# Kernel tuning notes

Measured on AMD Instinct MI355X. Metric: run time of the kernel, lower is better.

Reference implementation:

```python
import jax, jax.numpy as jnp
import numpy as np

N, E, B = 65536, 524288, 256
FEAT, EMB, NH, NB, NC = 64, 128, 4, 2, 4
OUT = EMB // NH
SLOPE = 0.01  # LeakyReLU negative_slope used everywhere in the module


def lrelu(x):
    return jnp.where(x > 0, x, SLOPE * x)


def seg_softmax(logits, seg, nseg, mask):
    # PyG softmax(src, batch): exp(x - segment_max) / (segment_sum + 1e-16)
    z = jnp.where(mask, logits, -jnp.inf)
    m = jax.ops.segment_max(z, seg, num_segments=nseg)
    m = jnp.where(jnp.isfinite(m), m, 0.0)
    e = jnp.exp(z - m[seg])
    s = jax.ops.segment_sum(e, seg, num_segments=nseg)
    return e / (s[seg] + 1e-16)


def topk_pool(x, seg, w, min_score, nseg):
    # PyG TopKPooling with min_score: score = softmax(x.w, batch);
    # keep nodes with score > min(min_score, per-graph max - 1e-7); x_out = x*score.
    score = x @ w  # [N]
    sm = seg_softmax(score, seg, nseg, jnp.ones(score.shape, bool))
    smax = jax.ops.segment_max(sm, seg, num_segments=nseg)
    thr = jnp.minimum(smax - 1e-7, min_score)
    keep = sm > thr[seg]
    xp = jnp.where(keep[:, None], x * sm[:, None], 0.0)
    return xp, keep


def graph_conv_max(x, src, dst, emask, Wrel, Wroot, b, n):
    # PyG GraphConv(aggr='max'): out = Wrel @ max_{j in N(i)} x_j + Wroot @ x_i + b
    msg = jnp.where(emask[:, None], x[src], -jnp.inf)  # [E, d]
    agg = jax.ops.segment_max(msg, dst, num_segments=n)
    agg = jnp.where(jnp.isfinite(agg), agg, 0.0)  # nodes with no in-edges -> 0 (PyG scatter fill)
    return agg @ Wrel.T + x @ Wroot.T + b


def batchnorm(x, g, b):
    # training-mode BatchNorm1d: batch statistics, biased variance, eps=1e-5
    mu = x.mean(0)
    var = x.var(0)
    return g * (x - mu) * jax.lax.rsqrt(var + 1e-5) + b


def setup_inputs() -> dict:
    key = jax.random.key(0)
    ks = jax.random.split(key, 16)
    s_feat = np.float32(1.0 / np.sqrt(FEAT))
    s_emb = np.float32(1.0 / np.sqrt(EMB))
    return {
        "x": jax.random.normal(ks[0], (N, FEAT), jnp.float32),
        "edge_index": jax.random.randint(ks[1], (2, E), 0, N, jnp.int32),
        "batch": (jnp.arange(N, dtype=jnp.int32) // (N // B)).astype(jnp.int32),
        "W_rel0": jax.random.normal(ks[2], (EMB, FEAT), jnp.float32) * s_feat,
        "W_root0": jax.random.normal(ks[3], (EMB, FEAT), jnp.float32) * s_feat,
        "b0": jnp.zeros((EMB,), jnp.float32),
        "bn0_g": jnp.ones((EMB,), jnp.float32),
        "bn0_b": jnp.zeros((EMB,), jnp.float32),
        "blk_pool_w": jax.random.normal(ks[4], (NB, NH, EMB), jnp.float32) * s_emb,
        "blk_Wrel": jax.random.normal(ks[5], (NB, NH, OUT, EMB), jnp.float32) * s_emb,
        "blk_Wroot": jax.random.normal(ks[6], (NB, NH, OUT, EMB), jnp.float32) * s_emb,
        "blk_b": jnp.zeros((NB, NH, OUT), jnp.float32),
        "blk_bn_g": jnp.ones((NB, EMB), jnp.float32),
        "blk_bn_b": jnp.zeros((NB, EMB), jnp.float32),
        "cls_pool_w": jax.random.normal(ks[7], (NC, EMB), jnp.float32) * s_emb,
        "cls_gW1": jax.random.normal(ks[8], (NC, EMB, EMB), jnp.float32) * s_emb,
        "cls_gb1": jnp.zeros((NC, EMB), jnp.float32),
        "cls_gW2": jax.random.normal(ks[9], (NC, EMB), jnp.float32) * s_emb,
        "cls_gb2": jnp.zeros((NC,), jnp.float32),
        "cls_fW1": jax.random.normal(ks[10], (NC, EMB, EMB), jnp.float32) * s_emb,
        "cls_fb1": jnp.zeros((NC, EMB), jnp.float32),
        "cls_fW2": jax.random.normal(ks[11], (NC, EMB), jnp.float32) * s_emb,
        "cls_fb2": jnp.zeros((NC,), jnp.float32),
        "batch_size": B,
    }


def reference(x, edge_index, batch, W_rel0, W_root0, b0, bn0_g, bn0_b,
              blk_pool_w, blk_Wrel, blk_Wroot, blk_b, blk_bn_g, blk_bn_b,
              cls_pool_w, cls_gW1, cls_gb1, cls_gW2, cls_gb2,
              cls_fW1, cls_fb1, cls_fW2, cls_fb2, batch_size):
    n = x.shape[0]
    src, dst = edge_index[0], edge_index[1]
    all_e = jnp.ones(src.shape, bool)
    # conv0 -> leaky_relu -> bn0
    h = lrelu(graph_conv_max(x, src, dst, all_e, W_rel0, W_root0, b0, n))
    cur = batchnorm(h, bn0_g, bn0_b)
    # multi-head blocks: pool (min_score=0.7) -> GraphConv(max) per head, scatter
    # back to original node slots, concat heads, bn, residual 0.5*(x + 0.5*bn(new))
    for bi in range(NB):
        heads = []
        for hi in range(NH):
            xp, keep = topk_pool(cur, batch, blk_pool_w[bi, hi], 0.7, batch_size)
            emask = keep[src] & keep[dst]
            o = lrelu(graph_conv_max(xp, src, dst, emask,
                                     blk_Wrel[bi, hi], blk_Wroot[bi, hi],
                                     blk_b[bi, hi], n))
            heads.append(jnp.where(keep[:, None], o, 0.0))
        new = batchnorm(jnp.concatenate(heads, axis=-1), blk_bn_g[bi], blk_bn_b[bi])
        cur = 0.5 * (cur + 0.5 * new)
    # classification heads: pool (min_score=0.8) -> GlobalAttention -> MLP -> 1
    outs = []
    for c in range(NC):
        xp, keep = topk_pool(cur, batch, cls_pool_w[c], 0.8, batch_size)
        gate = lrelu(xp @ cls_gW1[c].T + cls_gb1[c]) @ cls_gW2[c] + cls_gb2[c]  # [N]
        a = seg_softmax(gate, batch, batch_size, keep)
        pooled = jax.ops.segment_sum(a[:, None] * xp, batch, num_segments=batch_size)  # [B, EMB]
        y = lrelu(pooled @ cls_fW1[c].T + cls_fb1[c]) @ cls_fW2[c] + cls_fb2[c]  # [B]
        outs.append(y)
    logits = jnp.stack(outs, axis=-1)  # [B, NC]
    return jax.nn.log_softmax(logits, axis=-1)
```

## Files before the change

kernel.cpp:

```cpp
#include <hip/hip_runtime.h>
#include <math.h>

#define NN 65536
#define NE 524288
#define NG 256
#define SLOPE 0.01f

__device__ __forceinline__ float lrelu(float v){ return v > 0.f ? v : SLOPE*v; }

__device__ __forceinline__ float blockMax4(float v, float* s4){
  #pragma unroll
  for(int o=32;o>0;o>>=1) v = fmaxf(v, __shfl_down(v, o, 64));
  int t = threadIdx.x;
  __syncthreads();
  if((t&63)==0) s4[t>>6] = v;
  __syncthreads();
  return fmaxf(fmaxf(s4[0], s4[1]), fmaxf(s4[2], s4[3]));
}
__device__ __forceinline__ float blockSum4(float v, float* s4){
  #pragma unroll
  for(int o=32;o>0;o>>=1) v += __shfl_down(v, o, 64);
  int t = threadIdx.x;
  __syncthreads();
  if((t&63)==0) s4[t>>6] = v;
  __syncthreads();
  return (s4[0]+s4[1])+(s4[2]+s4[3]);
}

__global__ __launch_bounds__(256) void k_count(const int* __restrict__ ei, int* __restrict__ deg){
  int e = blockIdx.x*256 + threadIdx.x;
  if(e < NE) atomicAdd(&deg[ei[NE + e]], 1);
}

__global__ __launch_bounds__(1024) void k_scan(const int* __restrict__ deg,
      int* __restrict__ offs, int* __restrict__ cursor){
  __shared__ int part[1024];
  int t = threadIdx.x;
  int base = t*64;
  int s=0;
  for(int i=0;i<64;i++) s += deg[base+i];
  part[t]=s;
  __syncthreads();
  for(int off=1; off<1024; off<<=1){
    int v = (t>=off)? part[t-off] : 0;
    __syncthreads();
    part[t] += v;
    __syncthreads();
  }
  int run = (t==0)? 0 : part[t-1];
  for(int i=0;i<64;i++){
    int d = deg[base+i];
    offs[base+i] = run; cursor[base+i] = run;
    run += d;
  }
  if(t==1023) offs[NN] = run;
}

__global__ __launch_bounds__(256) void k_scatter(const int* __restrict__ ei,
      int* __restrict__ cursor, int* __restrict__ csr){
  int e = blockIdx.x*256 + threadIdx.x;
  if(e < NE){
    int d = ei[NE + e];
    int p = atomicAdd(&cursor[d], 1);
    csr[p] = ei[e];
  }
}

__global__ __launch_bounds__(256) void k_agg0(const float* __restrict__ x,
    const int* __restrict__ offs, const int* __restrict__ csr, float* __restrict__ agg0){
  int tid = blockIdx.x*256 + threadIdx.x;
  int node = tid>>4, q = tid&15;
  int e0 = offs[node], e1 = offs[node+1];
  float4 acc = make_float4(0.f,0.f,0.f,0.f);
  if(e0 < e1){
    acc = make_float4(-INFINITY,-INFINITY,-INFINITY,-INFINITY);
    int e = e0;
    for(; e+3 < e1; e += 4){
      int s0 = csr[e], s1 = csr[e+1], s2 = csr[e+2], s3 = csr[e+3];
      float4 v0 = ((const float4*)x)[s0*16 + q];
      float4 v1 = ((const float4*)x)[s1*16 + q];
      float4 v2 = ((const float4*)x)[s2*16 + q];
      float4 v3 = ((const float4*)x)[s3*16 + q];
      acc.x=fmaxf(acc.x,fmaxf(fmaxf(v0.x,v1.x),fmaxf(v2.x,v3.x)));
      acc.y=fmaxf(acc.y,fmaxf(fmaxf(v0.y,v1.y),fmaxf(v2.y,v3.y)));
      acc.z=fmaxf(acc.z,fmaxf(fmaxf(v0.z,v1.z),fmaxf(v2.z,v3.z)));
      acc.w=fmaxf(acc.w,fmaxf(fmaxf(v0.w,v1.w),fmaxf(v2.w,v3.w)));
    }
    for(; e < e1; e++){
      int s0 = csr[e];
      float4 v0 = ((const float4*)x)[s0*16 + q];
      acc.x=fmaxf(acc.x,v0.x); acc.y=fmaxf(acc.y,v0.y);
      acc.z=fmaxf(acc.z,v0.z); acc.w=fmaxf(acc.w,v0.w);
    }
  }
  ((float4*)agg0)[node*16 + q] = acc;
}

__global__ __launch_bounds__(256, 2) void k_conv0mm(
    const float* __restrict__ agg0, const float* __restrict__ x,
    const float* __restrict__ Wrel, const float* __restrict__ Wroot,
    const float* __restrict__ b0, float* __restrict__ cur,
    float* __restrict__ bnsum, float* __restrict__ bnsq){
  __shared__ float4 As[2048];
  __shared__ float4 Ws[2048];
  const int t = threadIdx.x;
  const int tn = t & 15;
  const int tc = t >> 4;
  float acc[8][8];
  #pragma unroll
  for(int i=0;i<8;i++)
    #pragma unroll
    for(int j=0;j<8;j++) acc[i][j]=0.f;

  const size_t tileoff = (size_t)blockIdx.x * 8192;
  #pragma unroll 1
  for(int ch=0; ch<2; ch++){
    const float4* gA = (const float4*)((ch==0? agg0 : x) + tileoff);
    const float4* gW = (const float4*)(ch==0? Wrel : Wroot);
    __syncthreads();
    #pragma unroll
    for(int i=0;i<8;i++){
      int idx = t + i*256;
      int n = idx>>4, k4 = idx&15;
      int sw = n*16 + ((k4 + (n>>3))&15);
      As[sw] = gA[idx];
      Ws[sw] = gW[idx];
    }
    __syncthreads();
    #pragma unroll 4
    for(int k4=0;k4<16;k4++){
      float4 a4[8], w4[8];
      #pragma unroll
      for(int i=0;i<8;i++) a4[i] = As[(tn*8+i)*16 + ((k4+tn)&15)];
      #pragma unroll
      for(int i=0;i<8;i++) w4[i] = Ws[(tc*8+i)*16 + ((k4+tc)&15)];
      #pragma unroll
      for(int i=0;i<8;i++)
        #pragma unroll
        for(int j=0;j<8;j++){
          acc[i][j] = fmaf(a4[i].x, w4[j].x, acc[i][j]);
          acc[i][j] = fmaf(a4[i].y, w4[j].y, acc[i][j]);
          acc[i][j] = fmaf(a4[i].z, w4[j].z, acc[i][j]);
          acc[i][j] = fmaf(a4[i].w, w4[j].w, acc[i][j]);
        }
    }
  }

  float bj[8];
  #pragma unroll
  for(int j=0;j<8;j++) bj[j] = b0[tc*8+j];
  float cs[8], cq[8];
  #pragma unroll
  for(int j=0;j<8;j++){ cs[j]=0.f; cq[j]=0.f; }
  const int nbase = blockIdx.x*128;
  #pragma unroll
  for(int i=0;i<8;i++){
    int node = nbase + tn*8 + i;
    float v[8];
    #pragma unroll
    for(int j=0;j<8;j++){
      v[j] = lrelu(acc[i][j] + bj[j]);
      cs[j] += v[j]; cq[j] += v[j]*v[j];
    }
    float4 o0 = make_float4(v[0],v[1],v[2],v[3]);
    float4 o1 = make_float4(v[4],v[5],v[6],v[7]);
    ((float4*)cur)[node*32 + tc*2 + 0] = o0;
    ((float4*)cur)[node*32 + tc*2 + 1] = o1;
  }
  __syncthreads();
  float* reds = (float*)As;
  float* redq = (float*)Ws;
  #pragma unroll
  for(int j=0;j<8;j++){
    reds[(tc*8+j)*16 + tn] = cs[j];
    redq[(tc*8+j)*16 + tn] = cq[j];
  }
  __syncthreads();
  if(t<128){
    float S=0.f, Q=0.f;
    #pragma unroll
    for(int i=0;i<16;i++){ S += reds[t*16+i]; Q += redq[t*16+i]; }
    atomicAdd(&bnsum[t], S);
    atomicAdd(&bnsq[t], Q);
  }
}

__global__ __launch_bounds__(256) void k_pool(const float* __restrict__ cur,
    const float* __restrict__ pw, float minscore,
    float* __restrict__ sm4, unsigned char* __restrict__ keep,
    int* __restrict__ cnt, int* __restrict__ wl,
    const float* __restrict__ bnsum, const float* __restrict__ bnsq,
    const float* __restrict__ gg, int fold){
  __shared__ __align__(16) float w[4][128];
  __shared__ float red[4];
  __shared__ float scv[128];
  int t = threadIdx.x, g = blockIdx.x;
  if(t<128){
    float sv = 1.f;
    if(fold){
      float mu = bnsum[t]*(1.0f/NN);
      float var = bnsq[t]*(1.0f/NN) - mu*mu;
      sv = gg[t]*rsqrtf(var+1e-5f);
    }
    scv[t] = sv;
  }
  __syncthreads();
  for(int i=t;i<512;i+=256) w[i>>7][i&127] = pw[i]*scv[i&127];
  __syncthreads();
  int n = g*256 + t;
  const float4* row = (const float4*)(cur + (size_t)n*128);
  float sc[4] = {0.f,0.f,0.f,0.f};
  for(int k=0;k<32;k++){
    float4 v = row[k];
    #pragma unroll
    for(int h=0;h<4;h++){
      const float4 wv = *(const float4*)&w[h][k*4];
      sc[h] += v.x*wv.x + v.y*wv.y + v.z*wv.z + v.w*wv.w;
    }
  }
  float4 smout;
  unsigned kb = 0;
  #pragma unroll 1
  for(int h=0;h<4;h++){
    float m = blockMax4(sc[h], red);
    float e = expf(sc[h]-m);
    float ssum = blockSum4(e, red);
    float sm = e/(ssum + 1e-16f);
    float smax = blockMax4(sm, red);
    float thr = fminf(smax - 1e-7f, minscore);
    ((float*)&smout)[h] = sm;
    if(sm > thr){
      kb |= (1u<<h);
      int p = atomicAdd(cnt, 1);
      wl[p] = (h<<16) | n;
    }
  }
  ((float4*)sm4)[n] = smout;
  keep[n] = (unsigned char)kb;
}

__global__ __launch_bounds__(256) void k_blockconv(const float* __restrict__ cur,
    const int* __restrict__ offs, const int* __restrict__ csr,
    const unsigned char* __restrict__ keep, const float* __restrict__ sm4,
    const int* __restrict__ cnt, const int* __restrict__ wl,
    const float* __restrict__ Wrel, const float* __restrict__ Wroot,
    const float* __restrict__ bias,
    float* __restrict__ onew, float* __restrict__ bnsum, float* __restrict__ bnsq,
    const float* __restrict__ bns0, const float* __restrict__ bnq0,
    const float* __restrict__ g0, const float* __restrict__ b0bn, int fold){
  __shared__ __align__(16) float aggs[8][128];
  __shared__ __align__(16) float xps[8][128];
  __shared__ __align__(16) float scv[128];
  __shared__ __align__(16) float ofv[128];
  const int t = threadIdx.x, grp = t>>5, lane = t&31;
  if(t<128){
    float sv = 1.f, ov = 0.f;
    if(fold){
      float mu = bns0[t]*(1.0f/NN);
      float var = bnq0[t]*(1.0f/NN) - mu*mu;
      sv = g0[t]*rsqrtf(var+1e-5f);
      ov = b0bn[t] - mu*sv;
    }
    scv[t]=sv; ofv[t]=ov;
  }
  __syncthreads();
  const float4 s4l = *(const float4*)&scv[lane*4];
  const float4 o4l = *(const float4*)&ofv[lane*4];
  const int total = *cnt;
  for(int item = blockIdx.x*8 + grp; item < total; item += gridDim.x*8){
    const int wv = wl[item];
    const int h = wv>>16, n = wv & 0xFFFF;
    const float smn = sm4[n*4+h];
    const int e0 = offs[n], e1 = offs[n+1];
    float4 acc = make_float4(-INFINITY,-INFINITY,-INFINITY,-INFINITY);
    bool any = false;
    for(int e=e0;e<e1;e++){
      int s = csr[e];
      if((keep[s]>>h)&1){
        any = true;
        float sv = sm4[s*4+h];
        float4 v = ((const float4*)cur)[s*32 + lane];
        v.x = (v.x*s4l.x + o4l.x)*sv; v.y = (v.y*s4l.y + o4l.y)*sv;
        v.z = (v.z*s4l.z + o4l.z)*sv; v.w = (v.w*s4l.w + o4l.w)*sv;
        acc.x = fmaxf(acc.x, v.x); acc.y = fmaxf(acc.y, v.y);
        acc.z = fmaxf(acc.z, v.z); acc.w = fmaxf(acc.w, v.w);
      }
    }
    if(!any) acc = make_float4(0.f,0.f,0.f,0.f);
    *(float4*)&aggs[grp][lane*4] = acc;
    float4 xv = ((const float4*)cur)[n*32 + lane];
    xv.x = (xv.x*s4l.x + o4l.x)*smn; xv.y = (xv.y*s4l.y + o4l.y)*smn;
    xv.z = (xv.z*s4l.z + o4l.z)*smn; xv.w = (xv.w*s4l.w + o4l.w)*smn;
    *(float4*)&xps[grp][lane*4] = xv;
    const float* Wr = Wrel  + (size_t)(h*32+lane)*128;
    const float* Wo = Wroot + (size_t)(h*32+lane)*128;
    float o = bias[h*32+lane];
    for(int k=0;k<32;k++){
      float4 a  = *(const float4*)&aggs[grp][k*4];
      float4 xx = *(const float4*)&xps[grp][k*4];
      float4 wr = ((const float4*)Wr)[k];
      float4 wo = ((const float4*)Wo)[k];
      o += a.x*wr.x + a.y*wr.y + a.z*wr.z + a.w*wr.w;
      o += xx.x*wo.x + xx.y*wo.y + xx.z*wo.z + xx.w*wo.w;
    }
    o = lrelu(o);
    onew[(size_t)n*128 + h*32 + lane] = o;
    atomicAdd(&bnsum[h*32+lane], o);
    atomicAdd(&bnsq[h*32+lane], o*o);
  }
}

__global__ __launch_bounds__(256) void k_updatepool(float* __restrict__ cur,
    const float* __restrict__ onew, const unsigned char* __restrict__ keepin,
    const float* __restrict__ bnsum, const float* __restrict__ bnsq,
    const float* __restrict__ gg, const float* __restrict__ bb,
    const float* __restrict__ bns0, const float* __restrict__ bnq0,
    const float* __restrict__ g0, const float* __restrict__ b0bn,
    const float* __restrict__ pw, float minscore,
    float* __restrict__ sm4, unsigned char* __restrict__ keepout,
    int* __restrict__ cnt, int* __restrict__ wl){
  __shared__ __align__(16) float sc1[128], of1[128], sc0[128], of0[128];
  __shared__ __align__(16) float w[4][128];
  __shared__ float red[4];
  const int t = threadIdx.x, g = blockIdx.x;
  if(t<128){
    float mu = bnsum[t]*(1.0f/NN);
    float var = bnsq[t]*(1.0f/NN) - mu*mu;
    float s = gg[t]*rsqrtf(var+1e-5f);
    sc1[t]=s; of1[t]=bb[t]-mu*s;
    float mu0 = bns0[t]*(1.0f/NN);
    float var0 = bnq0[t]*(1.0f/NN) - mu0*mu0;
    float s0v = g0[t]*rsqrtf(var0+1e-5f);
    sc0[t]=s0v; of0[t]=b0bn[t]-mu0*s0v;
  }
  for(int i=t;i<512;i+=256) w[i>>7][i&127] = pw[i];
  __syncthreads();
  const int n = g*256 + t;
  const unsigned kb_in = keepin[n];
  float sc[4] = {0.f,0.f,0.f,0.f};
  for(int k=0;k<32;k++){
    int h = k>>3;
    float4 v = ((const float4*)cur)[n*32 + k];
    float4 nv = make_float4(0.f,0.f,0.f,0.f);
    if((kb_in>>h)&1) nv = ((const float4*)onew)[n*32 + k];
    float4 s1 = *(const float4*)&sc1[k*4];
    float4 o1 = *(const float4*)&of1[k*4];
    float4 s0 = *(const float4*)&sc0[k*4];
    float4 o0 = *(const float4*)&of0[k*4];
    v.x = 0.5f*(s0.x*v.x + o0.x) + 0.25f*(s1.x*nv.x + o1.x);
    v.y = 0.5f*(s0.y*v.y + o0.y) + 0.25f*(s1.y*nv.y + o1.y);
    v.z = 0.5f*(s0.z*v.z + o0.z) + 0.25f*(s1.z*nv.z + o1.z);
    v.w = 0.5f*(s0.w*v.w + o0.w) + 0.25f*(s1.w*nv.w + o1.w);
    ((float4*)cur)[n*32 + k] = v;
    #pragma unroll
    for(int h2=0;h2<4;h2++){
      const float4 wv = *(const float4*)&w[h2][k*4];
      sc[h2] += v.x*wv.x + v.y*wv.y + v.z*wv.z + v.w*wv.w;
    }
  }
  float4 smout;
  unsigned kb = 0;
  #pragma unroll 1
  for(int h=0;h<4;h++){
    float m = blockMax4(sc[h], red);
    float e = expf(sc[h]-m);
    float ssum = blockSum4(e, red);
    float sm = e/(ssum + 1e-16f);
    float smax = blockMax4(sm, red);
    float thr = fminf(smax - 1e-7f, minscore);
    ((float*)&smout)[h] = sm;
    if(sm > thr){
      kb |= (1u<<h);
      int p = atomicAdd(cnt, 1);
      wl[p] = (h<<16) | n;
    }
  }
  ((float4*)sm4)[n] = smout;
  keepout[n] = (unsigned char)kb;
}

__global__ __launch_bounds__(256) void k_updatecls(float* __restrict__ cur,
    const float* __restrict__ onew, const unsigned char* __restrict__ keepin,
    const float* __restrict__ bnsum, const float* __restrict__ bnsq,
    const float* __restrict__ gg, const float* __restrict__ bb,
    const float* __restrict__ pw,
    const float* __restrict__ gW1, const float* __restrict__ gb1,
    const float* __restrict__ gW2, const float* __restrict__ gb2,
    const float* __restrict__ fW1, const float* __restrict__ fb1,
    const float* __restrict__ fW2, const float* __restrict__ fb2,
    float* __restrict__ out){
  __shared__ __align__(16) float sc1[128], of1[128];
  __shared__ __align__(16) float w[4][128];
  __shared__ float red[4];
  __shared__ int keptL[256];
  __shared__ float keptS[256];
  __shared__ float gateL[256];
  __shared__ __align__(16) float xk[128];
  __shared__ __align__(16) float pooled[128];
  __shared__ float yv[4];
  __shared__ int nkept;
  const int t = threadIdx.x, g = blockIdx.x;
  if(t<128){
    float mu = bnsum[t]*(1.0f/NN);
    float var = bnsq[t]*(1.0f/NN) - mu*mu;
    float s = gg[t]*rsqrtf(var+1e-5f);
    sc1[t]=s; of1[t]=bb[t]-mu*s;
  }
  for(int i=t;i<512;i+=256) w[i>>7][i&127] = pw[i];
  __syncthreads();
  const int n = g*256 + t;
  const unsigned kb_in = keepin[n];
  float sc4[4] = {0.f,0.f,0.f,0.f};
  for(int k=0;k<32;k++){
    int h = k>>3;
    float4 v = ((const float4*)cur)[n*32 + k];
    float4 nv = make_float4(0.f,0.f,0.f,0.f);
    if((kb_in>>h)&1) nv = ((const float4*)onew)[n*32 + k];
    float4 s1 = *(const float4*)&sc1[k*4];
    float4 o1 = *(const float4*)&of1[k*4];
    v.x = 0.5f*v.x + 0.25f*(s1.x*nv.x + o1.x);
    v.y = 0.5f*v.y + 0.25f*(s1.y*nv.y + o1.y);
    v.z = 0.5f*v.z + 0.25f*(s1.z*nv.z + o1.z);
    v.w = 0.5f*v.w + 0.25f*(s1.w*nv.w + o1.w);
    ((float4*)cur)[n*32 + k] = v;
    #pragma unroll
    for(int c=0;c<4;c++){
      const float4 wv = *(const float4*)&w[c][k*4];
      sc4[c] += v.x*wv.x + v.y*wv.y + v.z*wv.z + v.w*wv.w;
    }
  }
  __syncthreads();
  #pragma unroll 1
  for(int c=0;c<4;c++){
    float m = blockMax4(sc4[c], red);
    float e = expf(sc4[c]-m);
    float ssum = blockSum4(e, red);
    float sm = e/(ssum+1e-16f);
    float smax = blockMax4(sm, red);
    float thr = fminf(smax - 1e-7f, 0.8f);
    if(t==0) nkept = 0;
    __syncthreads();
    if(sm > thr){
      int p = atomicAdd(&nkept,1);
      keptL[p]=t; keptS[p]=sm;
    }
    __syncthreads();
    const int K = nkept;
    for(int k=0;k<K;k++){
      int ln = keptL[k]; float sv = keptS[k];
      if(t<32){
        float4 v = ((const float4*)(cur + (size_t)(g*256+ln)*128))[t];
        v.x*=sv; v.y*=sv; v.z*=sv; v.w*=sv;
        *(float4*)&xk[t*4] = v;
      }
      __syncthreads();
      float part = 0.f;
      if(t<128){
        const float* W = gW1 + (size_t)c*16384 + (size_t)t*128;
        float a = gb1[c*128+t];
        for(int f=0;f<32;f++){
          float4 xv = *(const float4*)&xk[f*4];
          float4 wv = ((const float4*)W)[f];
          a += xv.x*wv.x + xv.y*wv.y + xv.z*wv.z + xv.w*wv.w;
        }
        part = lrelu(a) * gW2[c*128+t];
      }
      float gs = blockSum4(part, red);
      if(t==0) gateL[k] = gs + gb2[c];
      __syncthreads();
    }
    float gv = (t<K)? gateL[t] : -INFINITY;
    float gm = blockMax4(gv, red);
    float ge = (t<K)? expf(gv-gm) : 0.f;
    float gsum = blockSum4(ge, red);
    if(t<K) gateL[t] = ge/(gsum+1e-16f);
    __syncthreads();
    if(t<128){
      float acc = 0.f;
      for(int k=0;k<K;k++)
        acc += gateL[k]*keptS[k]*cur[(size_t)(g*256+keptL[k])*128 + t];
      pooled[t]=acc;
    }
    __syncthreads();
    float part2=0.f;
    if(t<128){
      const float* F = fW1 + (size_t)c*16384 + (size_t)t*128;
      float a = fb1[c*128+t];
      for(int f=0;f<32;f++){
        float4 xv = *(const float4*)&pooled[f*4];
        float4 wv = ((const float4*)F)[f];
        a += xv.x*wv.x + xv.y*wv.y + xv.z*wv.z + xv.w*wv.w;
      }
      part2 = lrelu(a) * fW2[c*128+t];
    }
    float ysum = blockSum4(part2, red);
    if(t==0) yv[c] = ysum + fb2[c];
    __syncthreads();
  }
  if(t<4){
    float m = fmaxf(fmaxf(yv[0],yv[1]), fmaxf(yv[2],yv[3]));
    float l = logf(expf(yv[0]-m)+expf(yv[1]-m)+expf(yv[2]-m)+expf(yv[3]-m));
    out[g*4+t] = yv[t] - m - l;
  }
}

extern "C" void kernel_launch(void* const* d_in, const int* in_sizes, int n_in,
                              void* d_out, int out_size, void* d_ws, size_t ws_size,
                              hipStream_t stream){
  (void)in_sizes; (void)n_in; (void)out_size; (void)ws_size;
  const float* x     = (const float*)d_in[0];
  const int*   ei    = (const int*)d_in[1];
  const float* Wrel0 = (const float*)d_in[3];
  const float* Wroot0= (const float*)d_in[4];
  const float* b0    = (const float*)d_in[5];
  const float* bn0g  = (const float*)d_in[6];
  const float* bn0b  = (const float*)d_in[7];
  const float* bpw   = (const float*)d_in[8];
  const float* bWrel = (const float*)d_in[9];
  const float* bWroot= (const float*)d_in[10];
  const float* bbv   = (const float*)d_in[11];
  const float* bbng  = (const float*)d_in[12];
  const float* bbnb  = (const float*)d_in[13];
  const float* cpw   = (const float*)d_in[14];
  const float* gW1   = (const float*)d_in[15];
  const float* gb1   = (const float*)d_in[16];
  const float* gW2   = (const float*)d_in[17];
  const float* gb2   = (const float*)d_in[18];
  const float* fW1   = (const float*)d_in[19];
  const float* fb1   = (const float*)d_in[20];
  const float* fW2   = (const float*)d_in[21];
  const float* fb2   = (const float*)d_in[22];

  char* ws = (char*)d_ws;
  float* cur   = (float*)(ws + 0);
  float* onew  = (float*)(ws + 33554432ull);
  float* agg0  = onew;
  int*   csr   = (int*)(ws + 67108864ull);
  float* sm4   = (float*)(ws + 69206016ull);
  int*   wl    = (int*)(ws + 70254592ull);
  int*   offs  = (int*)(ws + 71303168ull);
  int*   cursor= (int*)(ws + 71565568ull);
  unsigned char* keep = (unsigned char*)(ws + 71827712ull);
  char*  Z     = ws + 71893248ull;
  int*   deg   = (int*)Z;
  float* bnsum0= (float*)(Z + 262144);
  float* bnsq0 = (float*)(Z + 262656);
  float* bnA   = (float*)(Z + 263168);
  float* bqA   = (float*)(Z + 263680);
  float* bnB   = (float*)(Z + 264192);
  float* bqB   = (float*)(Z + 264704);
  int*   cnt0  = (int*)(Z + 265216);
  int*   cnt1  = (int*)(Z + 265220);

  hipMemsetAsync(Z, 0, 265224, stream);

  k_count  <<<2048,256,0,stream>>>(ei, deg);
  k_scan   <<<1,1024,0,stream>>>(deg, offs, cursor);
  k_scatter<<<2048,256,0,stream>>>(ei, cursor, csr);

  k_agg0    <<<4096,256,0,stream>>>(x, offs, csr, agg0);
  k_conv0mm <<<512,256,0,stream>>>(agg0, x, Wrel0, Wroot0, b0, cur, bnsum0, bnsq0);

  k_pool     <<<256,256,0,stream>>>(cur, bpw, 0.7f, sm4, keep, cnt0, wl,
                                    bnsum0, bnsq0, bn0g, 1);
  k_blockconv<<<256,256,0,stream>>>(cur, offs, csr, keep, sm4, cnt0, wl,
                                    bWrel, bWroot, bbv, onew, bnA, bqA,
                                    bnsum0, bnsq0, bn0g, bn0b, 1);

  k_updatepool<<<256,256,0,stream>>>(cur, onew, keep, bnA, bqA, bbng, bbnb,
                                     bnsum0, bnsq0, bn0g, bn0b,
                                     bpw + 512, 0.7f, sm4, keep, cnt1, wl);

  k_blockconv<<<256,256,0,stream>>>(cur, offs, csr, keep, sm4, cnt1, wl,
                                    bWrel + 16384, bWroot + 16384, bbv + 128, onew, bnB, bqB,
                                    bnsum0, bnsq0, bn0g, bn0b, 0);

  k_updatecls<<<256,256,0,stream>>>(cur, onew, keep, bnB, bqB, bbng + 128, bbnb + 128,
                                    cpw, gW1, gb1, gW2, gb2, fW1, fb1, fW2, fb2,
                                    (float*)d_out);
}
```

Before: 443.5 us.

## Split pool/update kernels into wide streaming score pass plus per-graph selection

Replaces the per-node (one thread per 128-float row) update+score loops with a streaming kernel launched with 8192 blocks where each thread handles one float4, and the four head scores come from warp shuffle reductions. The segment softmax and top-k selection then run in a separate small kernel that reads the precomputed scores. The intent is coalesced memory access and far more parallelism than 256 blocks, which were bandwidth-starved with strided row reads. The cost is extra kernel launches and a scores round trip through global memory; the scores buffer aliases sm4, which k_poolsel reads and then overwrites, so an added __syncthreads guards that.

```diff
diff --git a/kernel.cpp b/kernel.cpp
--- a/kernel.cpp
+++ b/kernel.cpp
@@ -185,45 +185,90 @@
   }
 }
 
-__global__ __launch_bounds__(256) void k_pool(const float* __restrict__ cur,
-    const float* __restrict__ pw, float minscore,
-    float* __restrict__ sm4, unsigned char* __restrict__ keep,
-    int* __restrict__ cnt, int* __restrict__ wl,
-    const float* __restrict__ bnsum, const float* __restrict__ bnsq,
-    const float* __restrict__ gg, int fold){
+template<int MODE>
+__global__ __launch_bounds__(256) void k_stream(
+    float* __restrict__ cur, const float* __restrict__ onew,
+    const unsigned char* __restrict__ keepin,
+    const float* __restrict__ bnsA, const float* __restrict__ bnqA,
+    const float* __restrict__ g1, const float* __restrict__ b1,
+    const float* __restrict__ bns0, const float* __restrict__ bnq0,
+    const float* __restrict__ g0, const float* __restrict__ b0bn,
+    const float* __restrict__ pw, float* __restrict__ scores){
   __shared__ __align__(16) float w[4][128];
+  __shared__ __align__(16) float sc1[128], of1[128], sc0[128], of0[128];
+  const int t = threadIdx.x;
+  if(t<128){
+    if(MODE>=1){
+      float mu = bnsA[t]*(1.0f/NN);
+      float var = bnqA[t]*(1.0f/NN) - mu*mu;
+      float s = g1[t]*rsqrtf(var+1e-5f);
+      sc1[t]=s; of1[t]=b1[t]-mu*s;
+    }
+    if(MODE<=1){
+      float mu0 = bns0[t]*(1.0f/NN);
+      float var0 = bnq0[t]*(1.0f/NN) - mu0*mu0;
+      float s0 = g0[t]*rsqrtf(var0+1e-5f);
+      sc0[t]=s0; of0[t]=b0bn[t]-mu0*s0;
+    }
+  }
+  __syncthreads();
+  for(int i=t;i<512;i+=256){
+    float wv = pw[i];
+    if(MODE==0) wv *= sc0[i&127];
+    w[i>>7][i&127]=wv;
+  }
+  __syncthreads();
+  const int tid = blockIdx.x*256 + t;
+  const int n = tid>>5, k = tid&31;
+  float4 v = ((const float4*)cur)[tid];
+  if(MODE>=1){
+    const int h = k>>3;
+    float4 nv = make_float4(0.f,0.f,0.f,0.f);
+    if((keepin[n]>>h)&1) nv = ((const float4*)onew)[tid];
+    float4 s1 = *(const float4*)&sc1[k*4];
+    float4 o1 = *(const float4*)&of1[k*4];
+    if(MODE==1){
+      float4 s0 = *(const float4*)&sc0[k*4];
+      float4 o0 = *(const float4*)&of0[k*4];
+      v.x = 0.5f*(s0.x*v.x+o0.x) + 0.25f*(s1.x*nv.x+o1.x);
+      v.y = 0.5f*(s0.y*v.y+o0.y) + 0.25f*(s1.y*nv.y+o1.y);
+      v.z = 0.5f*(s0.z*v.z+o0.z) + 0.25f*(s1.z*nv.z+o1.z);
+      v.w = 0.5f*(s0.w*v.w+o0.w) + 0.25f*(s1.w*nv.w+o1.w);
+    } else {
+      v.x = 0.5f*v.x + 0.25f*(s1.x*nv.x+o1.x);
+      v.y = 0.5f*v.y + 0.25f*(s1.y*nv.y+o1.y);
+      v.z = 0.5f*v.z + 0.25f*(s1.z*nv.z+o1.z);
+      v.w = 0.5f*v.w + 0.25f*(s1.w*nv.w+o1.w);
+    }
+    ((float4*)cur)[tid] = v;
+  }
+  float sch[4];
+  #pragma unroll
+  for(int h2=0;h2<4;h2++){
+    float4 wv = *(const float4*)&w[h2][k*4];
+    sch[h2] = v.x*wv.x + v.y*wv.y + v.z*wv.z + v.w*wv.w;
+  }
+  #pragma unroll
+  for(int o=16;o>0;o>>=1){
+    #pragma unroll
+    for(int h2=0;h2<4;h2++) sch[h2] += __shfl_down(sch[h2], o, 32);
+  }
+  if(k==0) ((float4*)scores)[n] = make_float4(sch[0],sch[1],sch[2],sch[3]);
+}
+
+__global__ __launch_bounds__(256) void k_poolsel(const float* __restrict__ scores,
+    float minscore, float* __restrict__ sm4, unsigned char* __restrict__ keep,
+    int* __restrict__ cnt, int* __restrict__ wl){
   __shared__ float red[4];
-  __shared__ float scv[128];
-  int t = threadIdx.x, g = blockIdx.x;
-  if(t<128){
-    float sv = 1.f;
-    if(fold){
-      float mu = bnsum[t]*(1.0f/NN);
-      float var = bnsq[t]*(1.0f/NN) - mu*mu;
-      sv = gg[t]*rsqrtf(var+1e-5f);
-    }
-    scv[t] = sv;
-  }
-  __syncthreads();
-  for(int i=t;i<512;i+=256) w[i>>7][i&127] = pw[i]*scv[i&127];
-  __syncthreads();
-  int n = g*256 + t;
-  const float4* row = (const float4*)(cur + (size_t)n*128);
-  float sc[4] = {0.f,0.f,0.f,0.f};
-  for(int k=0;k<32;k++){
-    float4 v = row[k];
-    #pragma unroll
-    for(int h=0;h<4;h++){
-      const float4 wv = *(const float4*)&w[h][k*4];
-      sc[h] += v.x*wv.x + v.y*wv.y + v.z*wv.z + v.w*wv.w;
-    }
-  }
+  const int t = threadIdx.x, g = blockIdx.x, n = g*256 + t;
+  float4 s4 = ((const float4*)scores)[n];
+  float scv[4] = {s4.x, s4.y, s4.z, s4.w};
   float4 smout;
   unsigned kb = 0;
   #pragma unroll 1
   for(int h=0;h<4;h++){
-    float m = blockMax4(sc[h], red);
-    float e = expf(sc[h]-m);
+    float m = blockMax4(scv[h], red);
+    float e = expf(scv[h]-m);
     float ssum = blockSum4(e, red);
     float sm = e/(ssum + 1e-16f);
     float smax = blockMax4(sm, red);
@@ -235,6 +280,7 @@
       wl[p] = (h<<16) | n;
     }
   }
+  __syncthreads();
   ((float4*)sm4)[n] = smout;
   keep[n] = (unsigned char)kb;
 }
@@ -310,87 +356,13 @@
   }
 }
 
-__global__ __launch_bounds__(256) void k_updatepool(float* __restrict__ cur,
-    const float* __restrict__ onew, const unsigned char* __restrict__ keepin,
-    const float* __restrict__ bnsum, const float* __restrict__ bnsq,
-    const float* __restrict__ gg, const float* __restrict__ bb,
-    const float* __restrict__ bns0, const float* __restrict__ bnq0,
-    const float* __restrict__ g0, const float* __restrict__ b0bn,
-    const float* __restrict__ pw, float minscore,
-    float* __restrict__ sm4, unsigned char* __restrict__ keepout,
-    int* __restrict__ cnt, int* __restrict__ wl){
-  __shared__ __align__(16) float sc1[128], of1[128], sc0[128], of0[128];
-  __shared__ __align__(16) float w[4][128];
-  __shared__ float red[4];
-  const int t = threadIdx.x, g = blockIdx.x;
-  if(t<128){
-    float mu = bnsum[t]*(1.0f/NN);
-    float var = bnsq[t]*(1.0f/NN) - mu*mu;
-    float s = gg[t]*rsqrtf(var+1e-5f);
-    sc1[t]=s; of1[t]=bb[t]-mu*s;
-    float mu0 = bns0[t]*(1.0f/NN);
-    float var0 = bnq0[t]*(1.0f/NN) - mu0*mu0;
-    float s0v = g0[t]*rsqrtf(var0+1e-5f);
-    sc0[t]=s0v; of0[t]=b0bn[t]-mu0*s0v;
-  }
-  for(int i=t;i<512;i+=256) w[i>>7][i&127] = pw[i];
-  __syncthreads();
-  const int n = g*256 + t;
-  const unsigned kb_in = keepin[n];
-  float sc[4] = {0.f,0.f,0.f,0.f};
-  for(int k=0;k<32;k++){
-    int h = k>>3;
-    float4 v = ((const float4*)cur)[n*32 + k];
-    float4 nv = make_float4(0.f,0.f,0.f,0.f);
-    if((kb_in>>h)&1) nv = ((const float4*)onew)[n*32 + k];
-    float4 s1 = *(const float4*)&sc1[k*4];
-    float4 o1 = *(const float4*)&of1[k*4];
-    float4 s0 = *(const float4*)&sc0[k*4];
-    float4 o0 = *(const float4*)&of0[k*4];
-    v.x = 0.5f*(s0.x*v.x + o0.x) + 0.25f*(s1.x*nv.x + o1.x);
-    v.y = 0.5f*(s0.y*v.y + o0.y) + 0.25f*(s1.y*nv.y + o1.y);
-    v.z = 0.5f*(s0.z*v.z + o0.z) + 0.25f*(s1.z*nv.z + o1.z);
-    v.w = 0.5f*(s0.w*v.w + o0.w) + 0.25f*(s1.w*nv.w + o1.w);
-    ((float4*)cur)[n*32 + k] = v;
-    #pragma unroll
-    for(int h2=0;h2<4;h2++){
-      const float4 wv = *(const float4*)&w[h2][k*4];
-      sc[h2] += v.x*wv.x + v.y*wv.y + v.z*wv.z + v.w*wv.w;
-    }
-  }
-  float4 smout;
-  unsigned kb = 0;
-  #pragma unroll 1
-  for(int h=0;h<4;h++){
-    float m = blockMax4(sc[h], red);
-    float e = expf(sc[h]-m);
-    float ssum = blockSum4(e, red);
-    float sm = e/(ssum + 1e-16f);
-    float smax = blockMax4(sm, red);
-    float thr = fminf(smax - 1e-7f, minscore);
-    ((float*)&smout)[h] = sm;
-    if(sm > thr){
-      kb |= (1u<<h);
-      int p = atomicAdd(cnt, 1);
-      wl[p] = (h<<16) | n;
-    }
-  }
-  ((float4*)sm4)[n] = smout;
-  keepout[n] = (unsigned char)kb;
-}
-
-__global__ __launch_bounds__(256) void k_updatecls(float* __restrict__ cur,
-    const float* __restrict__ onew, const unsigned char* __restrict__ keepin,
-    const float* __restrict__ bnsum, const float* __restrict__ bnsq,
-    const float* __restrict__ gg, const float* __restrict__ bb,
-    const float* __restrict__ pw,
+__global__ __launch_bounds__(256) void k_cls(const float* __restrict__ cur,
+    const float* __restrict__ scores,
     const float* __restrict__ gW1, const float* __restrict__ gb1,
     const float* __restrict__ gW2, const float* __restrict__ gb2,
     const float* __restrict__ fW1, const float* __restrict__ fb1,
     const float* __restrict__ fW2, const float* __restrict__ fb2,
     float* __restrict__ out){
-  __shared__ __align__(16) float sc1[128], of1[128];
-  __shared__ __align__(16) float w[4][128];
   __shared__ float red[4];
   __shared__ int keptL[256];
   __shared__ float keptS[256];
@@ -400,36 +372,9 @@
   __shared__ float yv[4];
   __shared__ int nkept;
   const int t = threadIdx.x, g = blockIdx.x;
-  if(t<128){
-    float mu = bnsum[t]*(1.0f/NN);
-    float var = bnsq[t]*(1.0f/NN) - mu*mu;
-    float s = gg[t]*rsqrtf(var+1e-5f);
-    sc1[t]=s; of1[t]=bb[t]-mu*s;
-  }
-  for(int i=t;i<512;i+=256) w[i>>7][i&127] = pw[i];
-  __syncthreads();
   const int n = g*256 + t;
-  const unsigned kb_in = keepin[n];
-  float sc4[4] = {0.f,0.f,0.f,0.f};
-  for(int k=0;k<32;k++){
-    int h = k>>3;
-    float4 v = ((const float4*)cur)[n*32 + k];
-    float4 nv = make_float4(0.f,0.f,0.f,0.f);
-    if((kb_in>>h)&1) nv = ((const float4*)onew)[n*32 + k];
-    float4 s1 = *(const float4*)&sc1[k*4];
-    float4 o1 = *(const float4*)&of1[k*4];
-    v.x = 0.5f*v.x + 0.25f*(s1.x*nv.x + o1.x);
-    v.y = 0.5f*v.y + 0.25f*(s1.y*nv.y + o1.y);
-    v.z = 0.5f*v.z + 0.25f*(s1.z*nv.z + o1.z);
-    v.w = 0.5f*v.w + 0.25f*(s1.w*nv.w + o1.w);
-    ((float4*)cur)[n*32 + k] = v;
-    #pragma unroll
-    for(int c=0;c<4;c++){
-      const float4 wv = *(const float4*)&w[c][k*4];
-      sc4[c] += v.x*wv.x + v.y*wv.y + v.z*wv.z + v.w*wv.w;
-    }
-  }
-  __syncthreads();
+  float4 s4 = ((const float4*)scores)[n];
+  float sc4[4] = {s4.x, s4.y, s4.z, s4.w};
   #pragma unroll 1
   for(int c=0;c<4;c++){
     float m = blockMax4(sc4[c], red);
@@ -537,6 +482,7 @@
   float* agg0  = onew;
   int*   csr   = (int*)(ws + 67108864ull);
   float* sm4   = (float*)(ws + 69206016ull);
+  float* scores= sm4;
   int*   wl    = (int*)(ws + 70254592ull);
   int*   offs  = (int*)(ws + 71303168ull);
   int*   cursor= (int*)(ws + 71565568ull);
@@ -561,21 +507,25 @@
   k_agg0    <<<4096,256,0,stream>>>(x, offs, csr, agg0);
   k_conv0mm <<<512,256,0,stream>>>(agg0, x, Wrel0, Wroot0, b0, cur, bnsum0, bnsq0);
 
-  k_pool     <<<256,256,0,stream>>>(cur, bpw, 0.7f, sm4, keep, cnt0, wl,
-                                    bnsum0, bnsq0, bn0g, 1);
+  k_stream<0><<<8192,256,0,stream>>>(cur, onew, keep, bnA, bqA, bbng, bbnb,
+                                     bnsum0, bnsq0, bn0g, bn0b, bpw, scores);
+  k_poolsel<<<256,256,0,stream>>>(scores, 0.7f, sm4, keep, cnt0, wl);
+
   k_blockconv<<<256,256,0,stream>>>(cur, offs, csr, keep, sm4, cnt0, wl,
                                     bWrel, bWroot, bbv, onew, bnA, bqA,
                                     bnsum0, bnsq0, bn0g, bn0b, 1);
 
-  k_updatepool<<<256,256,0,stream>>>(cur, onew, keep, bnA, bqA, bbng, bbnb,
-                                     bnsum0, bnsq0, bn0g, bn0b,
-                                     bpw + 512, 0.7f, sm4, keep, cnt1, wl);
+  k_stream<1><<<8192,256,0,stream>>>(cur, onew, keep, bnA, bqA, bbng, bbnb,
+                                     bnsum0, bnsq0, bn0g, bn0b, bpw + 512, scores);
+  k_poolsel<<<256,256,0,stream>>>(scores, 0.7f, sm4, keep, cnt1, wl);
 
   k_blockconv<<<256,256,0,stream>>>(cur, offs, csr, keep, sm4, cnt1, wl,
                                     bWrel + 16384, bWroot + 16384, bbv + 128, onew, bnB, bqB,
                                     bnsum0, bnsq0, bn0g, bn0b, 0);
 
-  k_updatecls<<<256,256,0,stream>>>(cur, onew, keep, bnB, bqB, bbng + 128, bbnb + 128,
-                                    cpw, gW1, gb1, gW2, gb2, fW1, fb1, fW2, fb2,
-                                    (float*)d_out);
-}
+  k_stream<2><<<8192,256,0,stream>>>(cur, onew, keep, bnB, bqB, bbng + 128, bbnb + 128,
+                                     bnsum0, bnsq0, bn0g, bn0b, cpw, scores);
+
+  k_cls<<<256,256,0,stream>>>(cur, scores, gW1, gb1, gW2, gb2, fW1, fb1, fW2, fb2,
+                              (float*)d_out);
+}
```

Result: faster. 422.1 us (-4.8%).
